# Performance work log

Measured on AMD Instinct MI355X. Metric: run time of the kernel, lower is better.

## Reference

```python
import jax, jax.numpy as jnp
import numpy as np

COST_CLASS, COST_BBOX, COST_GIOU = 1.0, 5.0, 2.0
W_CE, W_BBOX, W_GIOU, W_DIFF = 1.0, 5.0, 2.0, 1.0
DIFFUSION_STEPS = 100


def box_cxcywh_to_xyxy(b):
    cx, cy, w, h = b[..., 0], b[..., 1], b[..., 2], b[..., 3]
    return jnp.stack([cx - 0.5 * w, cy - 0.5 * h, cx + 0.5 * w, cy + 0.5 * h], axis=-1)


def generalized_box_iou_pairwise(b1, b2):
    # b1: [N,4], b2: [M,4] in xyxy -> [N,M]
    area1 = (b1[:, 2] - b1[:, 0]) * (b1[:, 3] - b1[:, 1])
    area2 = (b2[:, 2] - b2[:, 0]) * (b2[:, 3] - b2[:, 1])
    lt = jnp.maximum(b1[:, None, :2], b2[None, :, :2])
    rb = jnp.minimum(b1[:, None, 2:], b2[None, :, 2:])
    wh = jnp.clip(rb - lt, 0.0)
    inter = wh[..., 0] * wh[..., 1]
    union = area1[:, None] + area2[None, :] - inter
    iou = inter / union
    lt_e = jnp.minimum(b1[:, None, :2], b2[None, :, :2])
    rb_e = jnp.maximum(b1[:, None, 2:], b2[None, :, 2:])
    wh_e = jnp.clip(rb_e - lt_e, 0.0)
    area_e = wh_e[..., 0] * wh_e[..., 1]
    return iou - (area_e - union) / area_e


def giou_elementwise(b1, b2):
    # b1, b2: [N,4] xyxy, aligned pairs (== diag of pairwise)
    area1 = (b1[:, 2] - b1[:, 0]) * (b1[:, 3] - b1[:, 1])
    area2 = (b2[:, 2] - b2[:, 0]) * (b2[:, 3] - b2[:, 1])
    lt = jnp.maximum(b1[:, :2], b2[:, :2])
    rb = jnp.minimum(b1[:, 2:], b2[:, 2:])
    wh = jnp.clip(rb - lt, 0.0)
    inter = wh[:, 0] * wh[:, 1]
    union = area1 + area2 - inter
    iou = inter / union
    lt_e = jnp.minimum(b1[:, :2], b2[:, :2])
    rb_e = jnp.maximum(b1[:, 2:], b2[:, 2:])
    wh_e = jnp.clip(rb_e - lt_e, 0.0)
    area_e = wh_e[:, 0] * wh_e[:, 1]
    return iou - (area_e - union) / area_e


def greedy_match(C):
    # C: [Q, T], T <= Q. Sequential argmin + row/col masking, T steps.
    Q, T = C.shape
    inf = jnp.array(jnp.inf, C.dtype)
    def step(Cm, _):
        idx = jnp.argmin(Cm)  # flat argmin, first-occurrence tie-break like numpy
        i, j = idx // T, idx % T
        Cm = Cm.at[i, :].set(inf).at[:, j].set(inf)
        return Cm, (i, j)
    _, (src, tgt) = jax.lax.scan(step, C, None, length=T)
    return src, tgt


def alphas_cumprod():
    betas = jnp.linspace(1e-4, 0.02, DIFFUSION_STEPS)
    return jnp.cumprod(1.0 - betas)


def _forward(pred_logits, pred_boxes, tgt_labels, tgt_boxes, tgt_time, noise):
    acp = alphas_cumprod()

    def per_image(logits, boxes, labels, tboxes, t, nz):
        # logits: [Q,C], boxes: [Q,4], labels: [T], tboxes: [T,4]
        prob = jax.nn.softmax(logits, axis=-1)
        cost_class = -prob[:, labels]                                   # [Q,T]
        cost_bbox = jnp.abs(boxes[:, None, :] - tboxes[None, :, :]).sum(-1)  # L1 cdist [Q,T]
        pb = box_cxcywh_to_xyxy(boxes)
        tb = box_cxcywh_to_xyxy(tboxes)
        cost_giou = -generalized_box_iou_pairwise(pb, tb)
        C = COST_CLASS * cost_class + COST_BBOX * cost_bbox + COST_GIOU * cost_giou
        src, tgt = greedy_match(jax.lax.stop_gradient(C))

        T = tboxes.shape[0]
        sel_logits = logits[src]                                        # [T,C]
        tgt_cls = labels[tgt]                                           # [T]
        logp = jax.nn.log_softmax(sel_logits, axis=-1)
        loss_ce = -jnp.take_along_axis(logp, tgt_cls[:, None], axis=1).mean()

        sb = boxes[src]
        gb = tboxes[tgt]
        loss_bbox = jnp.abs(sb - gb).sum() / T
        loss_giou = 1.0 - giou_elementwise(box_cxcywh_to_xyxy(sb), box_cxcywh_to_xyxy(gb)).mean()

        noise_scale = jnp.sqrt(1.0 - acp[t])
        noised_tgt = gb + nz[tgt] * noise_scale
        loss_diff = jnp.mean((sb - noised_tgt) ** 2)

        return (W_CE * loss_ce + W_BBOX * loss_bbox + W_GIOU * loss_giou + W_DIFF * loss_diff)

    per = jax.vmap(per_image)(pred_logits, pred_boxes, tgt_labels, tgt_boxes, tgt_time, noise)
    return per.mean()  # sum over batch / batch_size


def setup_inputs() -> dict:
    key = jax.random.key(0)
    k1, k2, k3, k4, k5, k6 = jax.random.split(key, 6)
    B, Q, C, T = 128, 500, 256, 100
    return {
        'pred_logits': jax.random.normal(k1, (B, Q, C), dtype=jnp.float32),
        'pred_boxes': jax.random.uniform(k2, (B, Q, 4), dtype=jnp.float32),
        'tgt_labels': jax.random.randint(k3, (B, T), 0, C, dtype=jnp.int32),
        'tgt_boxes': jax.random.uniform(k4, (B, T, 4), dtype=jnp.float32),
        'tgt_time': jax.random.randint(k5, (B,), 0, 100, dtype=jnp.int32),
        'noise': jax.random.normal(k6, (B, T, 4), dtype=jnp.float32),
    }


def reference(pred_logits, pred_boxes, tgt_labels, tgt_boxes, tgt_time, noise):
    return _forward(pred_logits, pred_boxes, tgt_labels, tgt_boxes, tgt_time, noise)
```

## Files before the change

### kernel.cpp

```cpp
#include <hip/hip_runtime.h>
#include <hip/hip_bf16.h>
#include <math.h>
#include <stdint.h>


#define QN 500
#define TN 100
#define CN 256
#define DIFFSTEPS 100
#define DEADKEY 0xFFFFFFFFFFFFFFFFull

__device__ __forceinline__ float giou_xyxy(float ax1, float ay1, float ax2, float ay2,
                                           float bx1, float by1, float bx2, float by2) {
    float area1 = (ax2 - ax1) * (ay2 - ay1);
    float area2 = (bx2 - bx1) * (by2 - by1);
    float ltx = fmaxf(ax1, bx1), lty = fmaxf(ay1, by1);
    float rbx = fminf(ax2, bx2), rby = fminf(ay2, by2);
    float w = fmaxf(rbx - ltx, 0.f), h = fmaxf(rby - lty, 0.f);
    float inter = w * h;
    float uni = area1 + area2 - inter;
    float iou = inter / uni;
    float ex1 = fminf(ax1, bx1), ey1 = fminf(ay1, by1);
    float ex2 = fmaxf(ax2, bx2), ey2 = fmaxf(ay2, by2);
    float ew = fmaxf(ex2 - ex1, 0.f), eh = fmaxf(ey2 - ey1, 0.f);
    float ae = ew * eh;
    return iou - (ae - uni) / ae;
}

__device__ __forceinline__ uint32_t fkey(float v) {
    uint32_t b = __float_as_uint(v);
    return (b & 0x80000000u) ? ~b : (b | 0x80000000u);
}

__device__ __forceinline__ unsigned long long packkey(float v, int flat) {
    return ((unsigned long long)fkey(v) << 32) | (unsigned long long)(uint32_t)flat;
}

__global__ __launch_bounds__(256) void cost_kernel(
    const float* __restrict__ logits, const float* __restrict__ boxes,
    const int* __restrict__ labels, const float* __restrict__ tboxes,
    float* __restrict__ Cmat, float* __restrict__ mxls) {

    const int wid = (blockIdx.x << 2) + (threadIdx.x >> 6);
    const int l   = threadIdx.x & 63;
    const int b   = wid / QN;

    const float* lrow = logits + (size_t)wid * CN;
    float4 lv = *(const float4*)(lrow + l * 4);

    float mx = fmaxf(fmaxf(lv.x, lv.y), fmaxf(lv.z, lv.w));
    #pragma unroll
    for (int o = 1; o < 64; o <<= 1) mx = fmaxf(mx, __shfl_xor(mx, o, 64));

    float se = expf(lv.x - mx) + expf(lv.y - mx) + expf(lv.z - mx) + expf(lv.w - mx);
    #pragma unroll
    for (int o = 1; o < 64; o <<= 1) se += __shfl_xor(se, o, 64);

    if (l == 0) mxls[wid] = mx + logf(se);
    float inv = 1.f / se;

    float4 pb = *(const float4*)(boxes + (size_t)wid * 4);
    float ax1 = pb.x - 0.5f * pb.z, ay1 = pb.y - 0.5f * pb.w;
    float ax2 = pb.x + 0.5f * pb.z, ay2 = pb.y + 0.5f * pb.w;

    #pragma unroll
    for (int half = 0; half < 2; ++half) {
        int t = half * 64 + l;
        bool valid = (t < TN);
        int cls = valid ? labels[b * TN + t] : 0;
        float4 tb = make_float4(0.f, 0.f, 0.f, 0.f);
        if (valid) tb = *(const float4*)(tboxes + ((size_t)b * TN + t) * 4);
        int sl = cls >> 2, ss = cls & 3;
        float g0 = __shfl(lv.x, sl, 64);
        float g1 = __shfl(lv.y, sl, 64);
        float g2 = __shfl(lv.z, sl, 64);
        float g3 = __shfl(lv.w, sl, 64);
        if (valid) {
            float lc = (ss == 0) ? g0 : (ss == 1) ? g1 : (ss == 2) ? g2 : g3;
            float e  = expf(lc - mx);
            float cc = -(e * inv);
            float cb = fabsf(pb.x - tb.x) + fabsf(pb.y - tb.y) +
                       fabsf(pb.z - tb.z) + fabsf(pb.w - tb.w);
            float bx1 = tb.x - 0.5f * tb.z, by1 = tb.y - 0.5f * tb.w;
            float bx2 = tb.x + 0.5f * tb.z, by2 = tb.y + 0.5f * tb.w;
            float g  = giou_xyxy(ax1, ay1, ax2, ay2, bx1, by1, bx2, by2);
            Cmat[(size_t)wid * TN + t] = cc + 5.f * cb - 2.f * g;
        }
    }
}

__global__ __launch_bounds__(128) void init_cols_kernel(
    const float* __restrict__ Cmat, unsigned long long* __restrict__ kcol) {
    const int b = blockIdx.x;
    const int t = threadIdx.x;
    if (t >= TN) return;
    const float* Cb = Cmat + (size_t)b * QN * TN;
    float bv = INFINITY; int ba = 0;
    for (int q = 0; q < QN; ++q) {
        float c = Cb[(size_t)q * TN + t];
        if (c < bv) { bv = c; ba = q; }
    }
    kcol[b * TN + t] = packkey(bv, ba * TN + t);
}

__global__ __launch_bounds__(64) void match_kernel(
    const float* __restrict__ logits, const float* __restrict__ boxes,
    const int* __restrict__ labels, const float* __restrict__ tboxes,
    const int* __restrict__ ttime, const float* __restrict__ noise,
    const float* __restrict__ Cmat, const unsigned long long* __restrict__ kcol,
    const float* __restrict__ mxls, float* __restrict__ per_img) {

    const int b = blockIdx.x;
    const int l = threadIdx.x;
    const float* Cb = Cmat + (size_t)b * QN * TN;

    unsigned long long kc0 = kcol[b * TN + l];
    unsigned long long kc1 = (l < TN - 64) ? kcol[b * TN + 64 + l] : DEADKEY;
    int ar0 = (int)((uint32_t)kc0) / TN;
    int ar1 = (kc1 != DEADKEY) ? (int)((uint32_t)kc1) / TN : -1;

    unsigned long long ra[8];
    #pragma unroll
    for (int m = 0; m < 8; ++m) ra[m] = ~0ull;
    ra[7] = (1ull << (QN - 448)) - 1;

    int pi0 = 0, pj0 = 0, pi1 = 0, pj1 = 0;

    for (int k = 0; k < TN; ++k) {
        unsigned long long pk = (kc0 < kc1) ? kc0 : kc1;
        #pragma unroll
        for (int o = 1; o < 64; o <<= 1) {
            unsigned long long q2 = __shfl_xor(pk, o, 64);
            pk = (q2 < pk) ? q2 : pk;
        }
        int flat = (int)(uint32_t)pk;
        int i = flat / TN;
        int j = flat - i * TN;

        if (k < 64) { if (l == k)      { pi0 = i; pj0 = j; } }
        else        { if (l == k - 64) { pi1 = i; pj1 = j; } }

        if (j < 64) { if (l == j)      kc0 = DEADKEY; }
        else        { if (l == j - 64) kc1 = DEADKEY; }

        int im = i >> 6; unsigned long long ib = 1ull << (i & 63);
        #pragma unroll
        for (int m = 0; m < 8; ++m) if (m == im) ra[m] &= ~ib;

        bool need0 = (kc0 != DEADKEY) && (ar0 == i);
        bool need1 = (kc1 != DEADKEY) && (ar1 == i);

        unsigned long long bal = __ballot(need0);
        while (bal) {
            int src = (int)__ffsll(bal) - 1;
            int jj = src;
            unsigned long long best = DEADKEY;
            #pragma unroll
            for (int m = 0; m < 8; ++m) {
                int q = m * 64 + l;
                if (((ra[m] >> l) & 1ull) != 0ull) {
                    float c = Cb[(size_t)q * TN + jj];
                    unsigned long long kk = packkey(c, q * TN + jj);
                    best = (kk < best) ? kk : best;
                }
            }
            #pragma unroll
            for (int o = 1; o < 64; o <<= 1) {
                unsigned long long q2 = __shfl_xor(best, o, 64);
                best = (q2 < best) ? q2 : best;
            }
            if (l == src) { kc0 = best; ar0 = (int)((uint32_t)best) / TN; }
            bal &= bal - 1;
        }
        bal = __ballot(need1);
        while (bal) {
            int src = (int)__ffsll(bal) - 1;
            int jj = 64 + src;
            unsigned long long best = DEADKEY;
            #pragma unroll
            for (int m = 0; m < 8; ++m) {
                int q = m * 64 + l;
                if (((ra[m] >> l) & 1ull) != 0ull) {
                    float c = Cb[(size_t)q * TN + jj];
                    unsigned long long kk = packkey(c, q * TN + jj);
                    best = (kk < best) ? kk : best;
                }
            }
            #pragma unroll
            for (int o = 1; o < 64; o <<= 1) {
                unsigned long long q2 = __shfl_xor(best, o, 64);
                best = (q2 < best) ? q2 : best;
            }
            if (l == src) { kc1 = best; ar1 = (int)((uint32_t)best) / TN; }
            bal &= bal - 1;
        }
    }

    int t = ttime[b];
    float step = (0.02f - 1e-4f) / (float)(DIFFSTEPS - 1);
    float acp = 1.f;
    for (int i2 = 0; i2 <= t; ++i2) acp *= (1.f - (1e-4f + step * (float)i2));
    float scale = sqrtf(1.f - acp);

    float contrib = 0.f;
    #pragma unroll
    for (int rnd = 0; rnd < 2; ++rnd) {
        int i = rnd ? pi1 : pi0, j = rnd ? pj1 : pj0;
        if (rnd == 0 || l < TN - 64) {
            int cls = labels[b * TN + j];
            float lc = logits[((size_t)b * QN + i) * CN + cls];
            float ce = mxls[b * QN + i] - lc;

            float4 sb = *(const float4*)(boxes + ((size_t)b * QN + i) * 4);
            float4 gb = *(const float4*)(tboxes + ((size_t)b * TN + j) * 4);
            float bb = fabsf(sb.x - gb.x) + fabsf(sb.y - gb.y) +
                       fabsf(sb.z - gb.z) + fabsf(sb.w - gb.w);

            float ax1 = sb.x - 0.5f * sb.z, ay1 = sb.y - 0.5f * sb.w;
            float ax2 = sb.x + 0.5f * sb.z, ay2 = sb.y + 0.5f * sb.w;
            float bx1 = gb.x - 0.5f * gb.z, by1 = gb.y - 0.5f * gb.w;
            float bx2 = gb.x + 0.5f * gb.z, by2 = gb.y + 0.5f * gb.w;
            float gi = giou_xyxy(ax1, ay1, ax2, ay2, bx1, by1, bx2, by2);

            float4 nz = *(const float4*)(noise + ((size_t)b * TN + j) * 4);
            float d0 = sb.x - (gb.x + nz.x * scale), d1 = sb.y - (gb.y + nz.y * scale);
            float d2 = sb.z - (gb.z + nz.z * scale), d3 = sb.w - (gb.w + nz.w * scale);
            float df = d0 * d0 + d1 * d1 + d2 * d2 + d3 * d3;

            contrib += ce + 5.f * bb - 2.f * gi + 0.25f * df;
        }
    }
    #pragma unroll
    for (int o = 1; o < 64; o <<= 1) contrib += __shfl_xor(contrib, o, 64);
    if (l == 0) per_img[b] = 2.0f + contrib / (float)TN;
}

__global__ void finalize_kernel(const float* __restrict__ per_img, float* __restrict__ out, int B) {
    __shared__ float red[256];
    int tid = threadIdx.x;
    float v = (tid < B) ? per_img[tid] : 0.f;
    red[tid] = v;
    __syncthreads();
    for (int s = 128; s > 0; s >>= 1) {
        if (tid < s) red[tid] += red[tid + s];
        __syncthreads();
    }
    if (tid == 0) out[0] = red[0] / (float)B;
}

extern "C" void kernel_launch(void* const* d_in, const int* in_sizes, int n_in,
                              void* d_out, int out_size, void* d_ws, size_t ws_size,
                              hipStream_t stream) {
    const float* pred_logits = (const float*)d_in[0];
    const float* pred_boxes  = (const float*)d_in[1];
    const int*   tgt_labels  = (const int*)d_in[2];
    const float* tgt_boxes   = (const float*)d_in[3];
    const int*   tgt_time    = (const int*)d_in[4];
    const float* noise       = (const float*)d_in[5];
    float* out = (float*)d_out;

    const int B = in_sizes[4];

    float* Cmat = (float*)d_ws;
    float* mxls = Cmat + (size_t)B * QN * TN;
    unsigned long long* kcol =
        (unsigned long long*)(mxls + (size_t)B * QN);
    float* per_img = (float*)(kcol + (size_t)B * TN);

    cost_kernel<<<(B * QN) / 4, 256, 0, stream>>>(
        pred_logits, pred_boxes, tgt_labels, tgt_boxes, Cmat, mxls);
    init_cols_kernel<<<B, 128, 0, stream>>>(Cmat, kcol);
    match_kernel<<<B, 64, 0, stream>>>(pred_logits, pred_boxes, tgt_labels,
                                       tgt_boxes, tgt_time, noise,
                                       Cmat, kcol, mxls, per_img);
    finalize_kernel<<<1, 256, 0, stream>>>(per_img, out, B);
}
```

Measured before the change: 241.7 us.

## Transpose cost matrix to column-major for coalesced column scans

The cost matrix is now stored as [B, T, Q] so that column rescans in the greedy matcher and the initial column argmin read contiguous memory. The column-init kernel is rewritten to use one wavefront per column with a shuffle reduction, which gives many more blocks than the old one-block-per-image serial loop. The rescan branches are also wrapped in a wave-wide any-check so the ballot work is skipped when no column needs a refresh. In exchange, the cost kernel's stores become strided across q (stride QN) instead of contiguous, which may hurt that kernel's write efficiency.

Result: no change. 241.8 us (+0.0%).

```diff
diff --git a/kernel.cpp b/kernel.cpp
--- a/kernel.cpp
+++ b/kernel.cpp
@@ -39,11 +39,12 @@
 __global__ __launch_bounds__(256) void cost_kernel(
     const float* __restrict__ logits, const float* __restrict__ boxes,
     const int* __restrict__ labels, const float* __restrict__ tboxes,
-    float* __restrict__ Cmat, float* __restrict__ mxls) {
+    float* __restrict__ CmatT, float* __restrict__ mxls) {
 
     const int wid = (blockIdx.x << 2) + (threadIdx.x >> 6);
     const int l   = threadIdx.x & 63;
     const int b   = wid / QN;
+    const int q   = wid - b * QN;
 
     const float* lrow = logits + (size_t)wid * CN;
     float4 lv = *(const float4*)(lrow + l * 4);
@@ -84,35 +85,45 @@
             float bx1 = tb.x - 0.5f * tb.z, by1 = tb.y - 0.5f * tb.w;
             float bx2 = tb.x + 0.5f * tb.z, by2 = tb.y + 0.5f * tb.w;
             float g  = giou_xyxy(ax1, ay1, ax2, ay2, bx1, by1, bx2, by2);
-            Cmat[(size_t)wid * TN + t] = cc + 5.f * cb - 2.f * g;
-        }
-    }
-}
-
-__global__ __launch_bounds__(128) void init_cols_kernel(
-    const float* __restrict__ Cmat, unsigned long long* __restrict__ kcol) {
-    const int b = blockIdx.x;
-    const int t = threadIdx.x;
-    if (t >= TN) return;
-    const float* Cb = Cmat + (size_t)b * QN * TN;
-    float bv = INFINITY; int ba = 0;
-    for (int q = 0; q < QN; ++q) {
-        float c = Cb[(size_t)q * TN + t];
-        if (c < bv) { bv = c; ba = q; }
-    }
-    kcol[b * TN + t] = packkey(bv, ba * TN + t);
+            CmatT[((size_t)b * TN + t) * QN + q] = cc + 5.f * cb - 2.f * g;
+        }
+    }
+}
+
+__global__ __launch_bounds__(256) void init_cols_kernel(
+    const float* __restrict__ CmatT, unsigned long long* __restrict__ kcol) {
+    const int wid = (blockIdx.x << 2) + (threadIdx.x >> 6);
+    const int l   = threadIdx.x & 63;
+    const int t   = wid % TN;
+
+    const float* col = CmatT + (size_t)wid * QN;
+    unsigned long long best = DEADKEY;
+    #pragma unroll
+    for (int m = 0; m < 8; ++m) {
+        int q = m * 64 + l;
+        if (q < QN) {
+            unsigned long long kk = packkey(col[q], q * TN + t);
+            best = (kk < best) ? kk : best;
+        }
+    }
+    #pragma unroll
+    for (int o = 1; o < 64; o <<= 1) {
+        unsigned long long q2 = __shfl_xor(best, o, 64);
+        best = (q2 < best) ? q2 : best;
+    }
+    if (l == 0) kcol[wid] = best;
 }
 
 __global__ __launch_bounds__(64) void match_kernel(
     const float* __restrict__ logits, const float* __restrict__ boxes,
     const int* __restrict__ labels, const float* __restrict__ tboxes,
     const int* __restrict__ ttime, const float* __restrict__ noise,
-    const float* __restrict__ Cmat, const unsigned long long* __restrict__ kcol,
+    const float* __restrict__ CmatT, const unsigned long long* __restrict__ kcol,
     const float* __restrict__ mxls, float* __restrict__ per_img) {
 
     const int b = blockIdx.x;
     const int l = threadIdx.x;
-    const float* Cb = Cmat + (size_t)b * QN * TN;
+    const float* CbT = CmatT + (size_t)b * TN * QN;
 
     unsigned long long kc0 = kcol[b * TN + l];
     unsigned long long kc1 = (l < TN - 64) ? kcol[b * TN + 64 + l] : DEADKEY;
@@ -150,49 +161,53 @@
         bool need0 = (kc0 != DEADKEY) && (ar0 == i);
         bool need1 = (kc1 != DEADKEY) && (ar1 == i);
 
-        unsigned long long bal = __ballot(need0);
-        while (bal) {
-            int src = (int)__ffsll(bal) - 1;
-            int jj = src;
-            unsigned long long best = DEADKEY;
-            #pragma unroll
-            for (int m = 0; m < 8; ++m) {
-                int q = m * 64 + l;
-                if (((ra[m] >> l) & 1ull) != 0ull) {
-                    float c = Cb[(size_t)q * TN + jj];
-                    unsigned long long kk = packkey(c, q * TN + jj);
-                    best = (kk < best) ? kk : best;
-                }
+        if (__any(need0 || need1)) {
+            unsigned long long bal = __ballot(need0);
+            while (bal) {
+                int src = (int)__ffsll(bal) - 1;
+                int jj = src;
+                const float* col = CbT + (size_t)jj * QN;
+                unsigned long long best = DEADKEY;
+                #pragma unroll
+                for (int m = 0; m < 8; ++m) {
+                    int q = m * 64 + l;
+                    if (((ra[m] >> l) & 1ull) != 0ull) {
+                        float c = col[q];
+                        unsigned long long kk = packkey(c, q * TN + jj);
+                        best = (kk < best) ? kk : best;
+                    }
+                }
+                #pragma unroll
+                for (int o = 1; o < 64; o <<= 1) {
+                    unsigned long long q2 = __shfl_xor(best, o, 64);
+                    best = (q2 < best) ? q2 : best;
+                }
+                if (l == src) { kc0 = best; ar0 = (int)((uint32_t)best) / TN; }
+                bal &= bal - 1;
             }
-            #pragma unroll
-            for (int o = 1; o < 64; o <<= 1) {
-                unsigned long long q2 = __shfl_xor(best, o, 64);
-                best = (q2 < best) ? q2 : best;
+            bal = __ballot(need1);
+            while (bal) {
+                int src = (int)__ffsll(bal) - 1;
+                int jj = 64 + src;
+                const float* col = CbT + (size_t)jj * QN;
+                unsigned long long best = DEADKEY;
+                #pragma unroll
+                for (int m = 0; m < 8; ++m) {
+                    int q = m * 64 + l;
+                    if (((ra[m] >> l) & 1ull) != 0ull) {
+                        float c = col[q];
+                        unsigned long long kk = packkey(c, q * TN + jj);
+                        best = (kk < best) ? kk : best;
+                    }
+                }
+                #pragma unroll
+                for (int o = 1; o < 64; o <<= 1) {
+                    unsigned long long q2 = __shfl_xor(best, o, 64);
+                    best = (q2 < best) ? q2 : best;
+                }
+                if (l == src) { kc1 = best; ar1 = (int)((uint32_t)best) / TN; }
+                bal &= bal - 1;
             }
-            if (l == src) { kc0 = best; ar0 = (int)((uint32_t)best) / TN; }
-            bal &= bal - 1;
-        }
-        bal = __ballot(need1);
-        while (bal) {
-            int src = (int)__ffsll(bal) - 1;
-            int jj = 64 + src;
-            unsigned long long best = DEADKEY;
-            #pragma unroll
-            for (int m = 0; m < 8; ++m) {
-                int q = m * 64 + l;
-                if (((ra[m] >> l) & 1ull) != 0ull) {
-                    float c = Cb[(size_t)q * TN + jj];
-                    unsigned long long kk = packkey(c, q * TN + jj);
-                    best = (kk < best) ? kk : best;
-                }
-            }
-            #pragma unroll
-            for (int o = 1; o < 64; o <<= 1) {
-                unsigned long long q2 = __shfl_xor(best, o, 64);
-                best = (q2 < best) ? q2 : best;
-            }
-            if (l == src) { kc1 = best; ar1 = (int)((uint32_t)best) / TN; }
-            bal &= bal - 1;
         }
     }
 
@@ -261,17 +276,17 @@
 
     const int B = in_sizes[4];
 
-    float* Cmat = (float*)d_ws;
-    float* mxls = Cmat + (size_t)B * QN * TN;
+    float* CmatT = (float*)d_ws;
+    float* mxls = CmatT + (size_t)B * QN * TN;
     unsigned long long* kcol =
         (unsigned long long*)(mxls + (size_t)B * QN);
     float* per_img = (float*)(kcol + (size_t)B * TN);
 
     cost_kernel<<<(B * QN) / 4, 256, 0, stream>>>(
-        pred_logits, pred_boxes, tgt_labels, tgt_boxes, Cmat, mxls);
-    init_cols_kernel<<<B, 128, 0, stream>>>(Cmat, kcol);
+        pred_logits, pred_boxes, tgt_labels, tgt_boxes, CmatT, mxls);
+    init_cols_kernel<<<(B * TN) / 4, 256, 0, stream>>>(CmatT, kcol);
     match_kernel<<<B, 64, 0, stream>>>(pred_logits, pred_boxes, tgt_labels,
                                        tgt_boxes, tgt_time, noise,
-                                       Cmat, kcol, mxls, per_img);
+                                       CmatT, kcol, mxls, per_img);
     finalize_kernel<<<1, 256, 0, stream>>>(per_img, out, B);
 }
```
